# Optimization experiments

Hardware: AMD Instinct MI355X
Metric: run time of the kernel (lower is better)

The kernel has to match this reference:

```python
import jax, jax.numpy as jnp
from jax import lax
import numpy as np

E = 8       # num experts
TOP_K = 2   # top-k routing
H = 84      # moe hidden size


def _maxpool2(x):
    # 2x2 max pool, stride 2, NCHW
    return lax.reduce_window(x, -jnp.inf, lax.max, (1, 1, 2, 2), (1, 1, 2, 2), 'VALID')


def setup_inputs() -> dict:
    key = jax.random.key(0)
    ks = jax.random.split(key, 16)
    N = 16384
    def lin(k, out_d, in_d, scale=None):
        s = scale if scale is not None else 1.0 / np.sqrt(in_d)
        return jax.random.uniform(k, (out_d, in_d), jnp.float32, -s, s)
    inp = {
        'x': jax.random.normal(ks[0], (N, 3, 32, 32), jnp.float32),
        'conv1_w': jax.random.normal(ks[1], (6, 3, 5, 5), jnp.float32) * (1.0 / np.sqrt(3 * 25)),
        'conv1_b': jnp.zeros((6,), jnp.float32),
        'conv2_w': jax.random.normal(ks[2], (16, 6, 5, 5), jnp.float32) * (1.0 / np.sqrt(6 * 25)),
        'conv2_b': jnp.zeros((16,), jnp.float32),
        'fc1_w': lin(ks[3], 120, 400),
        'fc1_b': jnp.zeros((120,), jnp.float32),
        'fc2_w': lin(ks[4], H, 120),
        'fc2_b': jnp.zeros((H,), jnp.float32),
        'gate_w': jax.random.normal(ks[5], (H, E), jnp.float32) * 0.02,
        'expert_w': jax.random.normal(ks[6], (E, H, H), jnp.float32) * (1.0 / np.sqrt(H)),  # [E, out, in]
        'expert_b': jnp.zeros((E, H), jnp.float32),
        'head_w': lin(ks[7], 10, H),
        'head_b': jnp.zeros((10,), jnp.float32),
    }
    return inp


def _forward(x, conv1_w, conv1_b, conv2_w, conv2_b, fc1_w, fc1_b,
             fc2_w, fc2_b, gate_w, expert_w, expert_b, head_w, head_b):
    dn = ('NCHW', 'OIHW', 'NCHW')
    # LeNet feature extractor
    h = lax.conv_general_dilated(x, conv1_w, (1, 1), 'VALID', dimension_numbers=dn)
    h = jax.nn.relu(h + conv1_b[None, :, None, None])          # [N,6,28,28]
    h = _maxpool2(h)                                           # [N,6,14,14]
    h = lax.conv_general_dilated(h, conv2_w, (1, 1), 'VALID', dimension_numbers=dn)
    h = jax.nn.relu(h + conv2_b[None, :, None, None])          # [N,16,10,10]
    h = _maxpool2(h)                                           # [N,16,5,5]
    h = h.reshape(h.shape[0], -1)                              # [N,400]
    # MLP hiddens
    h = jax.nn.relu(h @ fc1_w.T + fc1_b)                       # [N,120]
    h = jax.nn.relu(h @ fc2_w.T + fc2_b)                       # [N,84]
    # MoE layer: top-k softmax gating, expert Linear(84,84), weighted combine
    logits = h @ gate_w                                        # [N,E]
    probs = jax.nn.softmax(logits, axis=-1)
    top_v, top_i = lax.top_k(probs, TOP_K)                     # [N,k]
    top_v = top_v / jnp.sum(top_v, axis=-1, keepdims=True)     # renormalize top-k gates
    N = h.shape[0]
    combine = jnp.zeros((N, E), h.dtype).at[jnp.arange(N)[:, None], top_i].add(top_v)  # [N,E]
    expert_out = jnp.einsum('nd,eod->neo', h, expert_w) + expert_b[None]               # [N,E,84]
    h = jnp.einsum('ne,neo->no', combine, expert_out)          # [N,84]
    # head
    return h @ head_w.T + head_b                               # [N,10]


def reference(x, conv1_w, conv1_b, conv2_w, conv2_b, fc1_w, fc1_b,
              fc2_w, fc2_b, gate_w, expert_w, expert_b, head_w, head_b):
    return _forward(x, conv1_w, conv1_b, conv2_w, conv2_b, fc1_w, fc1_b,
                    fc2_w, fc2_b, gate_w, expert_w, expert_b, head_w, head_b)
```

## Files before the change

kernel.cpp:

```cpp
#include <hip/hip_runtime.h>
#include <math.h>

typedef _Float16 half8 __attribute__((ext_vector_type(8)));
typedef float f32x4 __attribute__((ext_vector_type(4)));

__device__ inline uint splitpack(float v) {
    _Float16 h = (_Float16)v;
    float r = v - (float)h;
    _Float16 l = (_Float16)r;
    return (uint)__builtin_bit_cast(unsigned short, h) |
           ((uint)__builtin_bit_cast(unsigned short, l) << 16);
}
__device__ inline _Float16 lo16h(uint u) { return __builtin_bit_cast(_Float16, (unsigned short)(u & 0xffffu)); }
__device__ inline _Float16 hi16h(uint u) { return __builtin_bit_cast(_Float16, (unsigned short)(u >> 16)); }
__device__ inline uint packhh(_Float16 a, _Float16 b) {
    return (uint)__builtin_bit_cast(unsigned short, a) |
           ((uint)__builtin_bit_cast(unsigned short, b) << 16);
}
__device__ inline float dpp_max8(float v) {
    int x = __builtin_amdgcn_mov_dpp(__builtin_bit_cast(int, v), 0x128, 0xf, 0xf, true);
    return fmaxf(v, __builtin_bit_cast(float, x));
}

__global__ __launch_bounds__(256) void k_conv1(const float* __restrict__ x,
                                               const float* __restrict__ w,
                                               const float* __restrict__ b,
                                               uint* __restrict__ p1) {
    __shared__ uint simg[6720];
    const int tid  = threadIdx.x;
    const int lane = tid & 63;
    const int wv   = tid >> 6;
    const int n0   = blockIdx.x * 2;

    const int colb = lane & 15;
    const int c  = colb & 7, dx = colb >> 3;
    const int g  = lane >> 4;
    const int qr = g;

    half8 bh[3], bl[3];
    #pragma unroll
    for (int ks = 0; ks < 3; ++ks)
        #pragma unroll
        for (int jj = 0; jj < 8; ++jj) {
            int pi = jj >> 1, e = jj & 1;
            int rho = g * 4 + pi;
            float val = 0.f;
            if (rho < 15 && c < 6) {
                int ci = rho / 5, ky = rho % 5;
                int kx = ks * 2 + e - dx;
                if (kx >= 0 && kx < 5) val = w[c * 75 + ci * 25 + ky * 5 + kx];
            }
            _Float16 hh = (_Float16)val;
            bh[ks][jj] = hh;
            bl[ks][jj] = (_Float16)(val - (float)hh);
        }
    const float bias = (c < 6) ? b[c] : 0.f;

    for (int i = tid; i < 1536; i += 256) {
        int im = i / 768;
        int rem = i - im * 768;
        int plane = rem >> 8, rr = (rem & 255) >> 3, f = rem & 7;
        float4 v = *(const float4*)(x + ((size_t)(n0 + im) * 3 + plane) * 1024 + rr * 32 + f * 4);
        _Float16 h0 = (_Float16)v.x, h1 = (_Float16)v.y, h2 = (_Float16)v.z, h3 = (_Float16)v.w;
        _Float16 l0 = (_Float16)(v.x - (float)h0), l1 = (_Float16)(v.y - (float)h1);
        _Float16 l2 = (_Float16)(v.z - (float)h2), l3 = (_Float16)(v.w - (float)h3);
        int base = im * 3360 + plane * 1120 + rr * 35 + f * 2;
        simg[base]      = packhh(h0, h1);
        simg[base + 1]  = packhh(h2, h3);
        simg[base + 16] = packhh(l0, l1);
        simg[base + 17] = packhh(l2, l3);
    }
    for (int i = tid; i < 168; i += 256) {
        int im = i / 84, rem = i % 84;
        int cc2 = rem / 14, y = rem % 14;
        p1[(size_t)(n0 + im) * 1260 + cc2 * 210 + y * 15 + 14] = 0u;
    }
    __syncthreads();

    int poff[4];
    #pragma unroll
    for (int pi = 0; pi < 4; ++pi) {
        int rho = g * 4 + pi;
        if (rho > 14) rho = 14;
        poff[pi] = (rho / 5) * 1120 + (rho % 5) * 35;
    }

    for (int t0 = wv; t0 < 50; t0 += 8) {
        const int t1 = (t0 + 4 < 50) ? (t0 + 4) : t0;
        const int im0 = (t0 >= 25) ? 1 : 0, tl0 = t0 - im0 * 25;
        const int im1 = (t1 >= 25) ? 1 : 0, tl1 = t1 - im1 * 25;
        int r0c = tl0 * 16 + colb; if (r0c > 391) r0c = 391;
        int r1c = tl1 * 16 + colb; if (r1c > 391) r1c = 391;
        int qx0 = (r0c * 586) >> 14, yy0 = r0c - qx0 * 28;
        int qx1 = (r1c * 586) >> 14, yy1 = r1c - qx1 * 28;
        const uint* base0 = simg + im0 * 3360 + yy0 * 35 + qx0;
        const uint* base1 = simg + im1 * 3360 + yy1 * 35 + qx1;

        f32x4 A0[2] = {{0.f,0.f,0.f,0.f},{0.f,0.f,0.f,0.f}};
        f32x4 A1[2] = {{0.f,0.f,0.f,0.f},{0.f,0.f,0.f,0.f}};
        int c0 = 0, c1 = 0;
        #pragma unroll
        for (int ks = 0; ks < 3; ++ks) {
            uint h0[4], l0[4], h1[4], l1[4];
            #pragma unroll
            for (int pi = 0; pi < 4; ++pi) {
                const uint* a0p = base0 + poff[pi];
                const uint* a1p = base1 + poff[pi];
                h0[pi] = a0p[ks];  l0[pi] = a0p[16 + ks];
                h1[pi] = a1p[ks];  l1[pi] = a1p[16 + ks];
            }
            uint4 hv0; hv0.x = h0[0]; hv0.y = h0[1]; hv0.z = h0[2]; hv0.w = h0[3];
            uint4 lv0; lv0.x = l0[0]; lv0.y = l0[1]; lv0.z = l0[2]; lv0.w = l0[3];
            uint4 hv1; hv1.x = h1[0]; hv1.y = h1[1]; hv1.z = h1[2]; hv1.w = h1[3];
            uint4 lv1; lv1.x = l1[0]; lv1.y = l1[1]; lv1.z = l1[2]; lv1.w = l1[3];
            half8 ah0 = __builtin_bit_cast(half8, hv0);
            half8 al0 = __builtin_bit_cast(half8, lv0);
            half8 ah1 = __builtin_bit_cast(half8, hv1);
            half8 al1 = __builtin_bit_cast(half8, lv1);
            A0[c0 & 1] = __builtin_amdgcn_mfma_f32_16x16x32_f16(ah0, bh[ks], A0[c0 & 1], 0, 0, 0); ++c0;
            A1[c1 & 1] = __builtin_amdgcn_mfma_f32_16x16x32_f16(ah1, bh[ks], A1[c1 & 1], 0, 0, 0); ++c1;
            A0[c0 & 1] = __builtin_amdgcn_mfma_f32_16x16x32_f16(ah0, bl[ks], A0[c0 & 1], 0, 0, 0); ++c0;
            A1[c1 & 1] = __builtin_amdgcn_mfma_f32_16x16x32_f16(ah1, bl[ks], A1[c1 & 1], 0, 0, 0); ++c1;
            A0[c0 & 1] = __builtin_amdgcn_mfma_f32_16x16x32_f16(al0, bh[ks], A0[c0 & 1], 0, 0, 0); ++c0;
            A1[c1 & 1] = __builtin_amdgcn_mfma_f32_16x16x32_f16(al1, bh[ks], A1[c1 & 1], 0, 0, 0); ++c1;
        }
        {
            f32x4 acc;
            #pragma unroll
            for (int i = 0; i < 4; ++i) acc[i] = A0[0][i] + A0[1][i];
            float p01 = dpp_max8(fmaxf(acc[0], acc[1]));
            float p23 = dpp_max8(fmaxf(acc[2], acc[3]));
            if (dx == 0 && c < 6) {
                uint* outb = p1 + (size_t)(n0 + im0) * 1260 + c * 210;
                int r0 = tl0 * 16 + qr * 4;
                if (r0 + 1 < 392) {
                    int qxa = (r0 * 586) >> 14, ya = r0 - qxa * 28;
                    outb[(ya >> 1) * 15 + qxa] = splitpack(fmaxf(p01 + bias, 0.f));
                }
                int r2 = r0 + 2;
                if (r2 + 1 < 392) {
                    int qxb = (r2 * 586) >> 14, yb = r2 - qxb * 28;
                    outb[(yb >> 1) * 15 + qxb] = splitpack(fmaxf(p23 + bias, 0.f));
                }
            }
        }
        if (t1 != t0) {
            f32x4 acc;
            #pragma unroll
            for (int i = 0; i < 4; ++i) acc[i] = A1[0][i] + A1[1][i];
            float p01 = dpp_max8(fmaxf(acc[0], acc[1]));
            float p23 = dpp_max8(fmaxf(acc[2], acc[3]));
            if (dx == 0 && c < 6) {
                uint* outb = p1 + (size_t)(n0 + im1) * 1260 + c * 210;
                int r0 = tl1 * 16 + qr * 4;
                if (r0 + 1 < 392) {
                    int qxa = (r0 * 586) >> 14, ya = r0 - qxa * 28;
                    outb[(ya >> 1) * 15 + qxa] = splitpack(fmaxf(p01 + bias, 0.f));
                }
                int r2 = r0 + 2;
                if (r2 + 1 < 392) {
                    int qxb = (r2 * 586) >> 14, yb = r2 - qxb * 28;
                    outb[(yb >> 1) * 15 + qxb] = splitpack(fmaxf(p23 + bias, 0.f));
                }
            }
        }
    }
}

__global__ __launch_bounds__(256) void k_conv2(const uint* __restrict__ p1,
                                               const float* __restrict__ w,
                                               const float* __restrict__ b,
                                               float* __restrict__ p2) {
    __shared__ __align__(16) uint simg[4 * 1260];
    const int tid  = threadIdx.x;
    const int lane = tid & 63;
    const int wv   = tid >> 6;
    const int n0   = blockIdx.x * 4;
    const int g  = lane >> 4;
    const int cc = lane & 15;
    const int qr = g;

    {
        const uint4* pg = (const uint4*)(p1 + (size_t)n0 * 1260);
        uint4* sg = (uint4*)simg;
        for (int i = tid; i < 1260; i += 256) sg[i] = pg[i];
    }

    half8 bh[6], bl[6];
    #pragma unroll
    for (int ks = 0; ks < 6; ++ks)
        #pragma unroll
        for (int jj = 0; jj < 8; ++jj) {
            int pi = jj >> 1, e = jj & 1;
            int rho = (ks / 3) * 16 + g * 4 + pi;
            int kx = (ks % 3) * 2 + e;
            float val = 0.f;
            if (rho < 30 && kx < 5) {
                int ci = rho / 5, ky = rho % 5;
                val = w[cc * 150 + ci * 25 + ky * 5 + kx];
            }
            _Float16 hh = (_Float16)val;
            bh[ks][jj] = hh;
            bl[ks][jj] = (_Float16)(val - (float)hh);
        }
    const float bias = b[cc];
    __syncthreads();

    int poff2[8];
    #pragma unroll
    for (int sp = 0; sp < 8; ++sp) {
        int sel = sp >> 2, pi = sp & 3;
        int rho = sel * 16 + g * 4 + pi;
        if (rho > 29) rho = 29;
        poff2[sp] = (rho / 5) * 210 + (rho % 5) * 15;
    }

    const uint* img = simg + wv * 1260;
    const int qw  = (lane & 15) >> 2;
    const int dy  = (lane >> 1) & 1, dxx = lane & 1;
    float* outb = p2 + (size_t)(n0 + wv) * 400 + cc * 25;

    for (int t = 0; t < 7; ++t) {
        int qa = t * 4 + qw; if (qa > 24) qa = 24;
        int qy = qa / 5, qx = qa % 5;
        int base = (2 * qy + dy) * 15 + (2 * qx + dxx);
        f32x4 acc2[2] = {{0.f,0.f,0.f,0.f},{0.f,0.f,0.f,0.f}};
        int pp = 0;
        #pragma unroll
        for (int sel = 0; sel < 2; ++sel) {
            uint P[4][6];
            #pragma unroll
            for (int pi = 0; pi < 4; ++pi) {
                const uint* ap = img + base + poff2[sel * 4 + pi];
                #pragma unroll
                for (int k = 0; k < 6; ++k) P[pi][k] = ap[k];
            }
            #pragma unroll
            for (int ksr = 0; ksr < 3; ++ksr) {
                const int ks = sel * 3 + ksr;
                uint hu[4], lu[4];
                #pragma unroll
                for (int pi = 0; pi < 4; ++pi) {
                    uint d0 = P[pi][ksr * 2], d1 = P[pi][ksr * 2 + 1];
                    hu[pi] = __builtin_amdgcn_perm(d1, d0, 0x05040100u);
                    lu[pi] = __builtin_amdgcn_perm(d1, d0, 0x07060302u);
                }
                uint4 hv; hv.x = hu[0]; hv.y = hu[1]; hv.z = hu[2]; hv.w = hu[3];
                uint4 lv; lv.x = lu[0]; lv.y = lu[1]; lv.z = lu[2]; lv.w = lu[3];
                half8 ah = __builtin_bit_cast(half8, hv);
                half8 al = __builtin_bit_cast(half8, lv);
                acc2[pp & 1] = __builtin_amdgcn_mfma_f32_16x16x32_f16(ah, bh[ks], acc2[pp & 1], 0, 0, 0); ++pp;
                acc2[pp & 1] = __builtin_amdgcn_mfma_f32_16x16x32_f16(ah, bl[ks], acc2[pp & 1], 0, 0, 0); ++pp;
                acc2[pp & 1] = __builtin_amdgcn_mfma_f32_16x16x32_f16(al, bh[ks], acc2[pp & 1], 0, 0, 0); ++pp;
            }
        }
        int qc = t * 4 + qr;
        if (qc < 25) {
            float m = fmaxf(fmaxf(acc2[0][0] + acc2[1][0], acc2[0][1] + acc2[1][1]),
                            fmaxf(acc2[0][2] + acc2[1][2], acc2[0][3] + acc2[1][3]));
            outb[qc] = fmaxf(m + bias, 0.f);
        }
    }
}

__global__ __launch_bounds__(256) void k_compose(const float* __restrict__ ew,
                                                 const float* __restrict__ eb,
                                                 const float* __restrict__ hw,
                                                 float* __restrict__ C,
                                                 float* __restrict__ hb2) {
    __shared__ float shw[840];
    __shared__ float seb[672];
    const int e = blockIdx.x, tid = threadIdx.x;
    for (int i = tid; i < 840; i += 256) shw[i] = hw[i];
    for (int i = tid; i < 672; i += 256) seb[i] = eb[i];
    __syncthreads();
    for (int i = tid; i < 840; i += 256) {
        int o = i / 84, d = i % 84;
        float s = 0.f;
        for (int j = 0; j < 84; ++j)
            s = fmaf(shw[o * 84 + j], ew[((size_t)e * 84 + j) * 84 + d], s);
        C[e * 840 + i] = s;
    }
    if (tid < 10) {
        float s = 0.f;
        for (int j = 0; j < 84; ++j) s = fmaf(shw[tid * 84 + j], seb[e * 84 + j], s);
        hb2[e * 10 + tid] = s;
    }
}

__global__ __launch_bounds__(512) void k_fc1tail(const float* __restrict__ p2,
                                                 const float* __restrict__ f1w,
                                                 const float* __restrict__ f1b,
                                                 const float* __restrict__ f2w,
                                                 const float* __restrict__ f2b,
                                                 const float* __restrict__ gw,
                                                 const float* __restrict__ Cw,
                                                 const float* __restrict__ hb2,
                                                 const float* __restrict__ headb,
                                                 float* __restrict__ out) {
    __shared__ float region[23872];
    __shared__ float sh1[7680];
    __shared__ float sfb[84];
    __shared__ int   sei[128];
    const int tid = threadIdx.x;
    const int n0 = blockIdx.x * 64;

    {
        float* sa  = region;
        float* swt = region + 6400;
        const int rg = tid >> 5;
        const int cg = tid & 31;
        float acc[4][4];
        #pragma unroll
        for (int i = 0; i < 4; ++i)
            #pragma unroll
            for (int j = 0; j < 4; ++j) acc[i][j] = 0.f;

        for (int kt = 0; kt < 4; ++kt) {
            __syncthreads();
            for (int i = tid; i < 1600; i += 512) {
                int r = i / 25, k4 = (i % 25) * 4;
                float4 v = *(const float4*)(p2 + (size_t)(n0 + r) * 400 + kt * 100 + k4);
                *(float4*)(sa + r * 100 + k4) = v;
            }
            for (int i = tid; i < 3000; i += 512) {
                int c = i / 25, k4 = (i % 25) * 4;
                float4 v = *(const float4*)(f1w + (size_t)c * 400 + kt * 100 + k4);
                float* d = swt + c * 101 + k4;
                d[0] = v.x; d[1] = v.y; d[2] = v.z; d[3] = v.w;
            }
            __syncthreads();
            if (cg < 30) {
                #pragma unroll 4
                for (int k = 0; k < 100; ++k) {
                    float av[4], wv[4];
                    #pragma unroll
                    for (int i = 0; i < 4; ++i) av[i] = sa[(rg * 4 + i) * 100 + k];
                    #pragma unroll
                    for (int j = 0; j < 4; ++j) wv[j] = swt[(cg * 4 + j) * 101 + k];
                    #pragma unroll
                    for (int i = 0; i < 4; ++i)
                        #pragma unroll
                        for (int j = 0; j < 4; ++j) acc[i][j] = fmaf(av[i], wv[j], acc[i][j]);
                }
            }
        }
        __syncthreads();
        if (cg < 30) {
            #pragma unroll
            for (int j = 0; j < 4; ++j) {
                const int o = cg * 4 + j;
                const float bo = f1b[o];
                #pragma unroll
                for (int i = 0; i < 4; ++i)
                    sh1[(rg * 4 + i) * 120 + o] = fmaxf(acc[i][j] + bo, 0.f);
            }
        }
    }

    float* sfw  = region;
    float* sC   = region + 10164;
    float* sh   = region + 16964;
    float* sgw  = region + 22404;
    float* shb2s= region + 23076;
    float* shb  = region + 23156;
    float* slog = region + 23168;
    float* swt2 = region + 23744;

    for (int i = tid; i < 2520; i += 512) {
        int o = i / 30, k4 = (i % 30) * 4;
        float4 v = *(const float4*)(f2w + (size_t)o * 120 + k4);
        float* d = sfw + o * 121 + k4;
        d[0] = v.x; d[1] = v.y; d[2] = v.z; d[3] = v.w;
    }
    for (int i = tid; i < 6720; i += 512) sC[(i / 84) * 85 + (i % 84)] = Cw[i];
    for (int i = tid; i < 672; i += 512) sgw[i] = gw[i];
    if (tid < 80) shb2s[tid] = hb2[tid];
    if (tid < 10) shb[tid] = headb[tid];
    if (tid < 84) sfb[tid] = f2b[tid];
    __syncthreads();

    for (int i = tid; i < 5376; i += 512) {
        const int t = i / 84, o = i % 84;
        const float* a = sh1 + t * 120;
        const float* wr = sfw + o * 121;
        float s = 0.f;
        #pragma unroll 8
        for (int k = 0; k < 120; ++k) s = fmaf(a[k], wr[k], s);
        sh[t * 85 + o] = fmaxf(s + sfb[o], 0.f);
    }
    __syncthreads();

    {
        const int t = tid / 8, e = tid % 8;
        const float* a = sh + t * 85;
        float s = 0.f;
        #pragma unroll 4
        for (int d = 0; d < 84; ++d) s = fmaf(a[d], sgw[d * 8 + e], s);
        slog[t * 9 + e] = s;
    }
    __syncthreads();

    if (tid < 64) {
        const float* l = slog + tid * 9;
        float m1 = l[0]; int i1 = 0;
        #pragma unroll
        for (int e = 1; e < 8; ++e) if (l[e] > m1) { m1 = l[e]; i1 = e; }
        float m2 = -1e30f; int i2 = 0;
        #pragma unroll
        for (int e = 0; e < 8; ++e) if (e != i1 && l[e] > m2) { m2 = l[e]; i2 = e; }
        const float r = expf(m2 - m1);
        const float inv = 1.f / (1.f + r);
        swt2[tid * 2] = inv; swt2[tid * 2 + 1] = r * inv;
        sei[tid * 2] = i1; sei[tid * 2 + 1] = i2;
    }
    __syncthreads();

    for (int i = tid; i < 640; i += 512) {
        const int t = i / 10, o = i % 10;
        const float* a = sh + t * 85;
        const float w0 = swt2[t * 2], w1 = swt2[t * 2 + 1];
        const int e0 = sei[t * 2], e1 = sei[t * 2 + 1];
        const float* c0 = sC + (e0 * 10 + o) * 85;
        const float* c1 = sC + (e1 * 10 + o) * 85;
        float s0 = 0.f, s1 = 0.f;
        #pragma unroll 4
        for (int d = 0; d < 84; ++d) {
            s0 = fmaf(a[d], c0[d], s0);
            s1 = fmaf(a[d], c1[d], s1);
        }
        out[(size_t)(n0 + t) * 10 + o] =
            shb[o] + w0 * (s0 + shb2s[e0 * 10 + o]) + w1 * (s1 + shb2s[e1 * 10 + o]);
    }
}

extern "C" void kernel_launch(void* const* d_in, const int* in_sizes, int n_in,
                              void* d_out, int out_size, void* d_ws, size_t ws_size,
                              hipStream_t stream) {
    const float* x   = (const float*)d_in[0];
    const float* c1w = (const float*)d_in[1];
    const float* c1b = (const float*)d_in[2];
    const float* c2w = (const float*)d_in[3];
    const float* c2b = (const float*)d_in[4];
    const float* f1w = (const float*)d_in[5];
    const float* f1b = (const float*)d_in[6];
    const float* f2w = (const float*)d_in[7];
    const float* f2b = (const float*)d_in[8];
    const float* gw  = (const float*)d_in[9];
    const float* ew  = (const float*)d_in[10];
    const float* eb  = (const float*)d_in[11];
    const float* hw  = (const float*)d_in[12];
    const float* hb  = (const float*)d_in[13];
    float* out = (float*)d_out;

    const int N = in_sizes[0] / 3072;

    float* ws = (float*)d_ws;
    uint*  p1  = (uint*)ws;
    float* p2  = ws + (size_t)N * 1260;
    float* C   = p2 + (size_t)N * 400;
    float* hb2 = C + 6720;

    k_conv1<<<N / 2, 256, 0, stream>>>(x, c1w, c1b, p1);
    k_conv2<<<N / 4, 256, 0, stream>>>(p1, c2w, c2b, p2);
    k_compose<<<8, 256, 0, stream>>>(ew, eb, hw, C, hb2);
    k_fc1tail<<<N / 64, 512, 0, stream>>>(p2, f1w, f1b, f2w, f2b, gw, C, hb2, hb, out);
}
```

Before: 294.0 us.

## Compute fc1 with split-fp16 MFMA instead of scalar FP32 FMAs

Replaces the scalar 4x4 register-tiled FP32 fc1 GEMM inside the fused tail kernel with MFMA 16x16x32 f16 instructions. Activations and weights are each split into high and low fp16 halves, and three MFMAs per tile approximate FP32 precision. Activations are staged in LDS as packed halves, and weights are read directly from global memory per wave. The sh1 row stride becomes 121 to reduce bank conflicts. This targets the fc1 FLOP cost, at the price of extra conversion work, a slightly lossy split-precision product, and uncached global weight reads.

```diff
diff --git a/kernel.cpp b/kernel.cpp
--- a/kernel.cpp
+++ b/kernel.cpp
@@ -298,62 +298,81 @@
                                                  const float* __restrict__ hb2,
                                                  const float* __restrict__ headb,
                                                  float* __restrict__ out) {
-    __shared__ float region[23872];
-    __shared__ float sh1[7680];
+    __shared__ __align__(16) float region[23872];
+    __shared__ float sh1[7744];
     __shared__ float sfb[84];
     __shared__ int   sei[128];
     const int tid = threadIdx.x;
     const int n0 = blockIdx.x * 64;
 
     {
-        float* sa  = region;
-        float* swt = region + 6400;
-        const int rg = tid >> 5;
-        const int cg = tid & 31;
-        float acc[4][4];
-        #pragma unroll
-        for (int i = 0; i < 4; ++i)
-            #pragma unroll
-            for (int j = 0; j < 4; ++j) acc[i][j] = 0.f;
-
-        for (int kt = 0; kt < 4; ++kt) {
+        uint* hplu = (uint*)region;
+        const int lane = tid & 63;
+        const int wvv  = tid >> 6;
+        const int cc = lane & 15, g = lane >> 4;
+        const int outg = wvv * 16 + cc;
+        f32x4 acc[4] = {{0.f,0.f,0.f,0.f},{0.f,0.f,0.f,0.f},{0.f,0.f,0.f,0.f},{0.f,0.f,0.f,0.f}};
+
+        for (int kc = 0; kc < 4; ++kc) {
             __syncthreads();
-            for (int i = tid; i < 1600; i += 512) {
-                int r = i / 25, k4 = (i % 25) * 4;
-                float4 v = *(const float4*)(p2 + (size_t)(n0 + r) * 400 + kt * 100 + k4);
-                *(float4*)(sa + r * 100 + k4) = v;
-            }
-            for (int i = tid; i < 3000; i += 512) {
-                int c = i / 25, k4 = (i % 25) * 4;
-                float4 v = *(const float4*)(f1w + (size_t)c * 400 + kt * 100 + k4);
-                float* d = swt + c * 101 + k4;
-                d[0] = v.x; d[1] = v.y; d[2] = v.z; d[3] = v.w;
+            for (int p = tid; p < 4096; p += 512) {
+                int row = p >> 6, pk = (p & 63) * 2;
+                int k = kc * 128 + pk;
+                float vx = 0.f, vy = 0.f;
+                if (k < 400) {
+                    float2 v = *(const float2*)(p2 + (size_t)(n0 + row) * 400 + k);
+                    vx = v.x; vy = v.y;
+                }
+                _Float16 h0 = (_Float16)vx, h1 = (_Float16)vy;
+                _Float16 l0 = (_Float16)(vx - (float)h0), l1 = (_Float16)(vy - (float)h1);
+                hplu[row * 68 + (pk >> 1)]        = packhh(h0, h1);
+                hplu[4352 + row * 68 + (pk >> 1)] = packhh(l0, l1);
             }
             __syncthreads();
-            if (cg < 30) {
-                #pragma unroll 4
-                for (int k = 0; k < 100; ++k) {
-                    float av[4], wv[4];
-                    #pragma unroll
-                    for (int i = 0; i < 4; ++i) av[i] = sa[(rg * 4 + i) * 100 + k];
-                    #pragma unroll
-                    for (int j = 0; j < 4; ++j) wv[j] = swt[(cg * 4 + j) * 101 + k];
-                    #pragma unroll
-                    for (int i = 0; i < 4; ++i)
-                        #pragma unroll
-                        for (int j = 0; j < 4; ++j) acc[i][j] = fmaf(av[i], wv[j], acc[i][j]);
+            const int nslice = (kc < 3) ? 4 : 1;
+            for (int s = 0; s < nslice; ++s) {
+                const int kbase = kc * 128 + s * 32 + g * 8;
+                float fa[8] = {0.f,0.f,0.f,0.f,0.f,0.f,0.f,0.f};
+                if (outg < 120 && kbase + 7 < 400) {
+                    float4 va = *(const float4*)(f1w + (size_t)outg * 400 + kbase);
+                    float4 vb = *(const float4*)(f1w + (size_t)outg * 400 + kbase + 4);
+                    fa[0]=va.x; fa[1]=va.y; fa[2]=va.z; fa[3]=va.w;
+                    fa[4]=vb.x; fa[5]=vb.y; fa[6]=vb.z; fa[7]=vb.w;
+                }
+                half8 ah, al;
+                #pragma unroll
+                for (int j = 0; j < 8; ++j) {
+                    _Float16 h = (_Float16)fa[j];
+                    ah[j] = h;
+                    al[j] = (_Float16)(fa[j] - (float)h);
+                }
+                #pragma unroll
+                for (int nt = 0; nt < 4; ++nt) {
+                    const int row = nt * 16 + cc;
+                    uint4 hv = *(const uint4*)(hplu + row * 68 + s * 16 + g * 4);
+                    uint4 lv = *(const uint4*)(hplu + 4352 + row * 68 + s * 16 + g * 4);
+                    half8 bh8 = __builtin_bit_cast(half8, hv);
+                    half8 bl8 = __builtin_bit_cast(half8, lv);
+                    acc[nt] = __builtin_amdgcn_mfma_f32_16x16x32_f16(ah, bh8, acc[nt], 0, 0, 0);
+                    acc[nt] = __builtin_amdgcn_mfma_f32_16x16x32_f16(ah, bl8, acc[nt], 0, 0, 0);
+                    acc[nt] = __builtin_amdgcn_mfma_f32_16x16x32_f16(al, bh8, acc[nt], 0, 0, 0);
                 }
             }
         }
         __syncthreads();
-        if (cg < 30) {
-            #pragma unroll
-            for (int j = 0; j < 4; ++j) {
-                const int o = cg * 4 + j;
-                const float bo = f1b[o];
-                #pragma unroll
-                for (int i = 0; i < 4; ++i)
-                    sh1[(rg * 4 + i) * 120 + o] = fmaxf(acc[i][j] + bo, 0.f);
+        float bo[4]; int ov[4];
+        #pragma unroll
+        for (int i2 = 0; i2 < 4; ++i2) {
+            ov[i2] = wvv * 16 + g * 4 + i2;
+            bo[i2] = (ov[i2] < 120) ? f1b[ov[i2]] : 0.f;
+        }
+        #pragma unroll
+        for (int nt = 0; nt < 4; ++nt) {
+            const int token = nt * 16 + cc;
+            #pragma unroll
+            for (int i2 = 0; i2 < 4; ++i2) {
+                if (ov[i2] < 120)
+                    sh1[token * 121 + ov[i2]] = fmaxf(acc[nt][i2] + bo[i2], 0.f);
             }
         }
     }
@@ -382,7 +401,7 @@
 
     for (int i = tid; i < 5376; i += 512) {
         const int t = i / 84, o = i % 84;
-        const float* a = sh1 + t * 120;
+        const float* a = sh1 + t * 121;
         const float* wr = sfw + o * 121;
         float s = 0.f;
         #pragma unroll 8
```

After: 268.3 us. 8.7% less time.
